# Optimization experiments

Measured on AMD Instinct MI355X. Metric: run time of the kernel, lower is better.

## Reference

```python
import jax, jax.numpy as jnp
import numpy as np

FEATURE_STRIDE = 16
CFG = {"TRAIN": dict(pre=12000, post=2000, thresh=0.7, min_size=16.0),
       "TEST":  dict(pre=6000,  post=300,  thresh=0.7, min_size=16.0)}

def _generate_anchors(base_size=16, ratios=(0.5, 1.0, 2.0), scales=(8, 16, 32)):
    xc = yc = (base_size - 1) * 0.5
    size = float(base_size * base_size)
    out = []
    for r in ratios:
        w = np.round(np.sqrt(size / r))
        h = np.round(w * r)
        for s in scales:
            W, H = w * s, h * s
            out.append([xc - 0.5 * (W - 1), yc - 0.5 * (H - 1),
                        xc + 0.5 * (W - 1), yc + 0.5 * (H - 1)])
    return np.array(out, np.float32)

ANCHORS = jnp.asarray(_generate_anchors())  # (9, 4)
NUM_ANCHORS = ANCHORS.shape[0]

def _pairwise_iou(b):
    x1, y1, x2, y2 = b[:, 0], b[:, 1], b[:, 2], b[:, 3]
    area = (x2 - x1 + 1.0) * (y2 - y1 + 1.0)
    iw = jnp.clip(jnp.minimum(x2[:, None], x2[None]) - jnp.maximum(x1[:, None], x1[None]) + 1.0, 0.0)
    ih = jnp.clip(jnp.minimum(y2[:, None], y2[None]) - jnp.maximum(y1[:, None], y1[None]) + 1.0, 0.0)
    inter = iw * ih
    return inter / (area[:, None] + area[None] - inter)

def _nms_keep(boxes, valid, thresh):
    # greedy NMS over score-sorted boxes; returns bool keep mask
    K = boxes.shape[0]
    iou = _pairwise_iou(boxes)  # (K, K)
    rng = jnp.arange(K)
    def body(i, keep):
        conflict = jnp.any((rng < i) & keep & (iou[i] > thresh))
        return keep.at[i].set(valid[i] & ~conflict)
    return jax.lax.fori_loop(0, K, body, jnp.zeros((K,), bool))

def reference(rpn_cls_scores, rpn_bbox_adjusts, img_shapes, train):
    cfg = CFG["TRAIN" if train else "TEST"]
    B, _, H, W = rpn_cls_scores.shape
    A = NUM_ANCHORS
    # fg scores: channels [A:2A], layout (h, w, a) after permute
    scores = rpn_cls_scores[:, A:].transpose(0, 2, 3, 1).reshape(B, -1)      # (B, N)
    deltas = rpn_bbox_adjusts.transpose(0, 2, 3, 1).reshape(B, -1, 4)        # (B, N, 4)
    # all anchors on the feature grid
    sx = jnp.arange(W, dtype=jnp.float32) * FEATURE_STRIDE
    sy = jnp.arange(H, dtype=jnp.float32) * FEATURE_STRIDE
    gy, gx = jnp.meshgrid(sy, sx, indexing="ij")
    shifts = jnp.stack([gx, gy, gx, gy], -1).reshape(-1, 4)                  # (H*W, 4)
    anchors = (shifts[:, None, :] + ANCHORS[None]).reshape(-1, 4)            # (N, 4)
    # bbox_transform_inv (+1 convention)
    aw = anchors[:, 2] - anchors[:, 0] + 1.0
    ah = anchors[:, 3] - anchors[:, 1] + 1.0
    acx = anchors[:, 0] + 0.5 * aw
    acy = anchors[:, 1] + 0.5 * ah
    pcx = deltas[..., 0] * aw + acx
    pcy = deltas[..., 1] * ah + acy
    pw = jnp.exp(deltas[..., 2]) * aw
    ph = jnp.exp(deltas[..., 3]) * ah
    x1, y1 = pcx - 0.5 * pw, pcy - 0.5 * ph
    x2, y2 = pcx + 0.5 * pw, pcy + 0.5 * ph
    imh, imw = img_shapes[:, 0:1], img_shapes[:, 1:2]
    x1 = jnp.clip(x1, 0.0, imw - 1.0); x2 = jnp.clip(x2, 0.0, imw - 1.0)
    y1 = jnp.clip(y1, 0.0, imh - 1.0); y2 = jnp.clip(y2, 0.0, imh - 1.0)
    boxes = jnp.stack([x1, y1, x2, y2], -1)                                  # (B, N, 4)
    valid = ((x2 - x1 + 1.0) >= cfg["min_size"]) & ((y2 - y1 + 1.0) >= cfg["min_size"])
    masked = jnp.where(valid, scores, -jnp.inf)
    K = min(cfg["pre"], boxes.shape[1])
    top_s, idx = jax.lax.top_k(masked, K)                                    # (B, K)
    top_b = jnp.take_along_axis(boxes, idx[..., None], axis=1)               # (B, K, 4)
    keep = jax.vmap(lambda b, v: _nms_keep(b, v, cfg["thresh"]))(
        jax.lax.stop_gradient(top_b), jnp.isfinite(top_s))
    post = cfg["post"]
    fin_s = jnp.where(keep, top_s, -jnp.inf)
    sel_s, idx2 = jax.lax.top_k(fin_s, post)
    sel_b = jnp.take_along_axis(top_b, idx2[..., None], axis=1)              # (B, post, 4)
    sel_b = jnp.where(jnp.isfinite(sel_s)[..., None], sel_b, 0.0)
    bix = jnp.broadcast_to(jnp.arange(B, dtype=sel_b.dtype)[:, None, None], (B, post, 1))
    return jnp.concatenate([bix, sel_b], -1)                                 # (B, post, 5)

def setup_inputs():
    key = jax.random.key(0)
    k1, k2 = jax.random.split(key)
    B, H, W = 4, 64, 96
    rpn_cls_scores = jax.random.normal(k1, (B, 2 * NUM_ANCHORS, H, W), jnp.float32)
    rpn_bbox_adjusts = jax.random.normal(k2, (B, 4 * NUM_ANCHORS, H, W), jnp.float32) * 0.1
    img_shapes = jnp.tile(jnp.array([[1024.0, 1536.0]], jnp.float32), (B, 1))
    return {"rpn_cls_scores": rpn_cls_scores, "rpn_bbox_adjusts": rpn_bbox_adjusts,
            "img_shapes": img_shapes, "train": 0}
```

## Files before the change

### kernel.cpp

```cpp
#include <hip/hip_runtime.h>


#define NB 4
#define AH 64
#define AW 96
#define NA 9
#define NPOS (AH*AW)
#define NPC (NPOS*NA)
#define CAP 16384
#define PREMAX 12000
#define POSTMAX 2048
#define HSZ 65536

__constant__ float c_anchors[NA][4] = {
  { -84.f,  -40.f,  99.f,  55.f},
  {-176.f,  -88.f, 191.f, 103.f},
  {-360.f, -184.f, 375.f, 199.f},
  { -56.f,  -56.f,  71.f,  71.f},
  {-120.f, -120.f, 135.f, 135.f},
  {-248.f, -248.f, 263.f, 263.f},
  { -36.f,  -80.f,  51.f,  95.f},
  { -80.f, -168.f,  95.f, 183.f},
  {-168.f, -344.f, 183.f, 359.f},
};

__device__ unsigned int       g_keys[NB][NPC];
__device__ float4             g_boxes[NB][NPC];
__device__ unsigned int       g_h16[NB][HSZ];
__device__ unsigned int       g_pivot[NB];
__device__ int                g_cnt[NB];
__device__ unsigned long long g_cand[NB][CAP];
__device__ int                g_cidx[NB][CAP];
__device__ int                g_rank[NB][CAP];
__device__ float4             g_sbox[NB][PREMAX];

__device__ __forceinline__ bool iou_gt(float4 a, float areaA, float4 q, float areaQ) {
#pragma clang fp contract(off)
  float iw = fminf(a.z, q.z) - fmaxf(a.x, q.x) + 1.0f; iw = fmaxf(iw, 0.0f);
  float ih = fminf(a.w, q.w) - fmaxf(a.y, q.y) + 1.0f; ih = fmaxf(ih, 0.0f);
  float inter = iw * ih;
  float denom = areaA + areaQ - inter;
  float d = inter - 0.7f * denom;
  if (__builtin_expect(fabsf(d) <= 4e-6f * denom, 0))
    return (inter / denom) > 0.7f;
  return d > 0.0f;
}

__global__ void __launch_bounds__(256) k_decode(const float* __restrict__ cls,
                                                const float* __restrict__ dlt,
                                                const float* __restrict__ ish) {
#pragma clang fp contract(off)
  int b   = blockIdx.y;
  int a   = blockIdx.x / (NPOS/256);
  int pos = (blockIdx.x % (NPOS/256)) * 256 + threadIdx.x;
  int wx  = pos % AW;
  int hy  = pos / AW;

  float score = cls[(b * (2*NA) + NA + a) * NPOS + pos];
  const float* dp = dlt + (b * (4*NA) + a*4) * NPOS + pos;
  float d0 = dp[0];
  float d1 = dp[NPOS];
  float d2 = dp[2*NPOS];
  float d3 = dp[3*NPOS];

  float shx = (float)(wx * 16);
  float shy = (float)(hy * 16);
  float ax1 = c_anchors[a][0] + shx;
  float ay1 = c_anchors[a][1] + shy;
  float ax2 = c_anchors[a][2] + shx;
  float ay2 = c_anchors[a][3] + shy;

  float aw_ = ax2 - ax1 + 1.0f;
  float ah_ = ay2 - ay1 + 1.0f;
  float acx = ax1 + 0.5f * aw_;
  float acy = ay1 + 0.5f * ah_;

  float pcx = d0 * aw_ + acx;
  float pcy = d1 * ah_ + acy;
  float pw  = expf(d2) * aw_;
  float ph  = expf(d3) * ah_;

  float x1 = pcx - 0.5f * pw;
  float y1 = pcy - 0.5f * ph;
  float x2 = pcx + 0.5f * pw;
  float y2 = pcy + 0.5f * ph;

  float imh = ish[b*2 + 0];
  float imw = ish[b*2 + 1];
  x1 = fminf(fmaxf(x1, 0.0f), imw - 1.0f);
  x2 = fminf(fmaxf(x2, 0.0f), imw - 1.0f);
  y1 = fminf(fmaxf(y1, 0.0f), imh - 1.0f);
  y2 = fminf(fmaxf(y2, 0.0f), imh - 1.0f);

  bool valid = ((x2 - x1 + 1.0f) >= 16.0f) && ((y2 - y1 + 1.0f) >= 16.0f);

  int i2 = a * NPOS + pos;
  g_boxes[b][i2] = make_float4(x1, y1, x2, y2);

  unsigned int key = 0u;
  if (valid) {
    unsigned int ub = __float_as_uint(score);
    key = (ub >> 31) ? ~ub : (ub | 0x80000000u);
  }
  g_keys[b][i2] = key;
  atomicAdd(&g_h16[b][key >> 16], 1u);
}

__global__ void __launch_bounds__(256) k_pivot(const int* __restrict__ train) {
  int b = blockIdx.x;
  int tid = threadIdx.x;
  unsigned int pre = train[0] ? 12000u : 6000u;
  const int CH = HSZ / 256;
  __shared__ unsigned int csum[256];
  __shared__ unsigned int csuf[257];
  __shared__ int best;

  uint4* hp = (uint4*)&g_h16[b][tid * CH];
  unsigned int s = 0;
#pragma unroll
  for (int q = 0; q < CH/4; ++q) { uint4 v = hp[q]; s += v.x + v.y + v.z + v.w; }
  csum[tid] = s;
  if (tid == 0) { best = 0; g_cnt[b] = 0; }
  __syncthreads();
  if (tid == 0) {
    unsigned int run = 0;
    csuf[256] = 0;
    for (int c = 255; c >= 0; --c) { run += csum[c]; csuf[c] = run; }
  }
  __syncthreads();

  unsigned int run = csuf[tid + 1];
  int loc = 0;
  for (int q = CH - 1; q >= 0; --q) {
    run += g_h16[b][tid * CH + q];
    if (loc == 0 && run >= pre) {
      int T = tid * CH + q;
      if (T >= 1) loc = T;
    }
  }
  uint4 z = make_uint4(0u, 0u, 0u, 0u);
#pragma unroll
  for (int q = 0; q < CH/4; ++q) hp[q] = z;

  if (loc) atomicMax(&best, loc);
  __syncthreads();
  if (tid == 0)
    g_pivot[b] = best ? ((unsigned int)best << 16) : 1u;
}

__global__ void __launch_bounds__(256) k_compact() {
  int b = blockIdx.y;
  int a   = blockIdx.x / (NPOS/256);
  int pos = (blockIdx.x % (NPOS/256)) * 256 + threadIdx.x;
  int i2 = a * NPOS + pos;
  unsigned int key = g_keys[b][i2];
  if (key >= g_pivot[b]) {
    int p = atomicAdd(&g_cnt[b], 1);
    if (p < CAP) {
      unsigned int iref = (unsigned int)(pos * NA + a);
      g_cand[b][p] = ((unsigned long long)key << 32) |
                     (unsigned long long)(0xFFFFFFFFu - iref);
      g_cidx[b][p] = i2;
    }
  }
}

__global__ void __launch_bounds__(256) k_rank() {
  int tid = threadIdx.x;
  __shared__ unsigned long long tl[256];
  for (int b = 0; b < NB; ++b) {
    int Cb = g_cnt[b]; if (Cb > CAP) Cb = CAP;
    int nt = (Cb + 255) >> 8;
    int tiles = nt * nt;
    for (int t = blockIdx.x; t < tiles; t += gridDim.x) {
      int jt = t / nt, kt = t - jt * nt;
      int k = kt * 256 + tid;
      tl[tid] = (k < Cb) ? g_cand[b][k] : 0ull;
      __syncthreads();
      int j = jt * 256 + tid;
      unsigned long long cj = (j < Cb) ? g_cand[b][j] : ~0ull;
      int r = 0;
#pragma unroll 8
      for (int q = 0; q < 256; ++q) r += (int)(tl[q] > cj);
      if (j < Cb && r) atomicAdd(&g_rank[b][j], r);
      __syncthreads();
    }
  }
}

__global__ void __launch_bounds__(512)
k_nms(float* __restrict__ out, const int* __restrict__ train, int post) {
#pragma clang fp contract(off)
  int b = blockIdx.x;
  int tid = threadIdx.x;
  int lane = tid & 63;
  int wid = tid >> 6;
  int pre = train[0] ? 12000 : 6000;
  int Cb = g_cnt[b]; if (Cb > CAP) Cb = CAP;
  int Kb = min(pre, Cb);

  for (int j = tid; j < Cb; j += 512) {
    int r = g_rank[b][j];
    g_rank[b][j] = 0;
    if (r < pre) {
      int i2 = g_cidx[b][j];
      g_sbox[b][r] = g_boxes[b][i2];
    }
  }
  __threadfence_block();
  __syncthreads();

  __shared__ float4 kbox[POSTMAX];
  __shared__ float  kar [POSTMAX];
  __shared__ float4 cbox[64];
  __shared__ float  car [64];
  __shared__ unsigned long long sup8[8];
  __shared__ unsigned long long conf8[8][64];
  __shared__ int s_nk;
  if (tid == 0) s_nk = 0;
  __syncthreads();
  int nk = 0;

  unsigned long long laneBitsBelow = (lane == 0) ? 0ull : (~0ull >> (64 - lane));

  for (int base = 0; base < Kb; base += 64) {
    int c = base + lane;
    bool active = (c < Kb);
    float4 bx = active ? g_sbox[b][c] : make_float4(0.f, 0.f, -1.f, -1.f);
    float area = (bx.z - bx.x + 1.0f) * (bx.w - bx.y + 1.0f);
    if (wid == 0) { cbox[lane] = bx; car[lane] = area; }

    int supp = active ? 0 : 1;
    {
      int t = wid;
      for (; t + 24 < nk; t += 32) {
        supp |= (int)iou_gt(bx, area, kbox[t],    kar[t]);
        supp |= (int)iou_gt(bx, area, kbox[t+8],  kar[t+8]);
        supp |= (int)iou_gt(bx, area, kbox[t+16], kar[t+16]);
        supp |= (int)iou_gt(bx, area, kbox[t+24], kar[t+24]);
      }
      for (; t < nk; t += 8) supp |= (int)iou_gt(bx, area, kbox[t], kar[t]);
    }
    unsigned long long myb = __ballot(supp);
    if (lane == 0) sup8[wid] = myb;
    __syncthreads();

    {
      unsigned long long confp = 0ull;
#pragma unroll
      for (int q = 0; q < 8; ++q) {
        int j = wid * 8 + q;
        if (iou_gt(bx, area, cbox[j], car[j])) confp |= (1ull << j);
      }
      conf8[wid][lane] = confp;
    }
    __syncthreads();

    if (wid == 0) {
      unsigned long long conf = (conf8[0][lane] | conf8[1][lane] |
                                 conf8[2][lane] | conf8[3][lane] |
                                 conf8[4][lane] | conf8[5][lane] |
                                 conf8[6][lane] | conf8[7][lane]) & laneBitsBelow;
      unsigned long long supAll = sup8[0] | sup8[1] | sup8[2] | sup8[3] |
                                  sup8[4] | sup8[5] | sup8[6] | sup8[7];
      unsigned long long pending = ~supAll;
      unsigned long long keptmask = 0ull;
      while (pending) {
        int i = __ffsll(pending) - 1;
        keptmask |= (1ull << i);
        unsigned long long confb = __ballot((int)((conf >> i) & 1ull));
        pending &= ~confb;
        pending &= ~(1ull << i);
      }
      int myPos = nk + __popcll(keptmask & laneBitsBelow);
      if (((keptmask >> lane) & 1ull) && myPos < post) {
        kbox[myPos] = bx;
        kar [myPos] = area;
        float* o = out + ((size_t)b * post + myPos) * 5;
        o[0] = (float)b; o[1] = bx.x; o[2] = bx.y; o[3] = bx.z; o[4] = bx.w;
      }
      if (lane == 0) s_nk = nk + __popcll(keptmask);
    }
    __syncthreads();
    nk = s_nk;
    if (nk >= post) break;
  }

  nk = min(nk, post);
  for (int r = nk + tid; r < post; r += 512) {
    float* o = out + ((size_t)b * post + r) * 5;
    o[0] = (float)b; o[1] = 0.0f; o[2] = 0.0f; o[3] = 0.0f; o[4] = 0.0f;
  }
}

extern "C" void kernel_launch(void* const* d_in, const int* in_sizes, int n_in,
                              void* d_out, int out_size, void* d_ws, size_t ws_size,
                              hipStream_t stream) {
  const float* cls   = (const float*)d_in[0];
  const float* dlt   = (const float*)d_in[1];
  const float* ish   = (const float*)d_in[2];
  const int*   train = (const int*)d_in[3];
  float* out = (float*)d_out;

  int post = out_size / (NB * 5);

  dim3 gdec(NA * (NPOS/256), NB);
  k_decode<<<gdec, 256, 0, stream>>>(cls, dlt, ish);

  k_pivot<<<NB, 256, 0, stream>>>(train);

  k_compact<<<gdec, 256, 0, stream>>>();

  k_rank<<<1024, 256, 0, stream>>>();

  k_nms<<<NB, 512, 0, stream>>>(out, train, post);
}
```

Before: 195.8 us.

## Fuse all proposal stages into one persistent kernel with grid barriers

Replaces the five launches (decode, pivot, compact, rank, NMS) with a single persistent kernel of 256 blocks of 1024 threads that move between stages through global atomic spin barriers. Alongside this, the histogram shrinks from 16 to 15 bits, the rank tiles grow, and NMS runs with 16 waves while the next 64-box chunk is prefetched. The aim is to remove launch gaps and widen the NMS stage. The risks are deadlock if all 256 blocks are not co-resident, the cost of the spin barriers themselves, and a serial NMS tail that still runs on only four blocks.

```diff
diff --git a/kernel.cpp b/kernel.cpp
--- a/kernel.cpp
+++ b/kernel.cpp
@@ -10,7 +10,12 @@
 #define CAP 16384
 #define PREMAX 12000
 #define POSTMAX 2048
-#define HSZ 65536
+#define HBITS 15
+#define HSZ (1<<HBITS)
+#define HSH (32-HBITS)
+#define NBLK 256
+#define NTHR 1024
+#define UNITS (NB*NA*(NPOS/NTHR))
 
 __constant__ float c_anchors[NA][4] = {
   { -84.f,  -40.f,  99.f,  55.f},
@@ -26,13 +31,26 @@
 
 __device__ unsigned int       g_keys[NB][NPC];
 __device__ float4             g_boxes[NB][NPC];
-__device__ unsigned int       g_h16[NB][HSZ];
+__device__ unsigned int       g_h15[NB][HSZ];
 __device__ unsigned int       g_pivot[NB];
 __device__ int                g_cnt[NB];
 __device__ unsigned long long g_cand[NB][CAP];
 __device__ int                g_cidx[NB][CAP];
 __device__ int                g_rank[NB][CAP];
 __device__ float4             g_sbox[NB][PREMAX];
+__device__ unsigned int       g_bar[8];
+
+__device__ __forceinline__ void gbar(int k) {
+  __syncthreads();
+  if (threadIdx.x == 0) {
+    __threadfence();
+    atomicAdd(&g_bar[k], 1u);
+    while (atomicAdd(&g_bar[k], 0u) < (unsigned)NBLK)
+      __builtin_amdgcn_s_sleep(8);
+    __threadfence();
+  }
+  __syncthreads();
+}
 
 __device__ __forceinline__ bool iou_gt(float4 a, float areaA, float4 q, float areaQ) {
 #pragma clang fp contract(off)
@@ -46,256 +64,295 @@
   return d > 0.0f;
 }
 
-__global__ void __launch_bounds__(256) k_decode(const float* __restrict__ cls,
-                                                const float* __restrict__ dlt,
-                                                const float* __restrict__ ish) {
+__global__ void __launch_bounds__(NTHR)
+k_all(const float* __restrict__ cls, const float* __restrict__ dlt,
+      const float* __restrict__ ish, const int* __restrict__ train,
+      float* __restrict__ out, int post) {
 #pragma clang fp contract(off)
-  int b   = blockIdx.y;
-  int a   = blockIdx.x / (NPOS/256);
-  int pos = (blockIdx.x % (NPOS/256)) * 256 + threadIdx.x;
-  int wx  = pos % AW;
-  int hy  = pos / AW;
-
-  float score = cls[(b * (2*NA) + NA + a) * NPOS + pos];
-  const float* dp = dlt + (b * (4*NA) + a*4) * NPOS + pos;
-  float d0 = dp[0];
-  float d1 = dp[NPOS];
-  float d2 = dp[2*NPOS];
-  float d3 = dp[3*NPOS];
-
-  float shx = (float)(wx * 16);
-  float shy = (float)(hy * 16);
-  float ax1 = c_anchors[a][0] + shx;
-  float ay1 = c_anchors[a][1] + shy;
-  float ax2 = c_anchors[a][2] + shx;
-  float ay2 = c_anchors[a][3] + shy;
-
-  float aw_ = ax2 - ax1 + 1.0f;
-  float ah_ = ay2 - ay1 + 1.0f;
-  float acx = ax1 + 0.5f * aw_;
-  float acy = ay1 + 0.5f * ah_;
-
-  float pcx = d0 * aw_ + acx;
-  float pcy = d1 * ah_ + acy;
-  float pw  = expf(d2) * aw_;
-  float ph  = expf(d3) * ah_;
-
-  float x1 = pcx - 0.5f * pw;
-  float y1 = pcy - 0.5f * ph;
-  float x2 = pcx + 0.5f * pw;
-  float y2 = pcy + 0.5f * ph;
-
-  float imh = ish[b*2 + 0];
-  float imw = ish[b*2 + 1];
-  x1 = fminf(fmaxf(x1, 0.0f), imw - 1.0f);
-  x2 = fminf(fmaxf(x2, 0.0f), imw - 1.0f);
-  y1 = fminf(fmaxf(y1, 0.0f), imh - 1.0f);
-  y2 = fminf(fmaxf(y2, 0.0f), imh - 1.0f);
-
-  bool valid = ((x2 - x1 + 1.0f) >= 16.0f) && ((y2 - y1 + 1.0f) >= 16.0f);
-
-  int i2 = a * NPOS + pos;
-  g_boxes[b][i2] = make_float4(x1, y1, x2, y2);
-
-  unsigned int key = 0u;
-  if (valid) {
-    unsigned int ub = __float_as_uint(score);
-    key = (ub >> 31) ? ~ub : (ub | 0x80000000u);
-  }
-  g_keys[b][i2] = key;
-  atomicAdd(&g_h16[b][key >> 16], 1u);
-}
-
-__global__ void __launch_bounds__(256) k_pivot(const int* __restrict__ train) {
-  int b = blockIdx.x;
-  int tid = threadIdx.x;
-  unsigned int pre = train[0] ? 12000u : 6000u;
-  const int CH = HSZ / 256;
-  __shared__ unsigned int csum[256];
-  __shared__ unsigned int csuf[257];
-  __shared__ int best;
-
-  uint4* hp = (uint4*)&g_h16[b][tid * CH];
-  unsigned int s = 0;
-#pragma unroll
-  for (int q = 0; q < CH/4; ++q) { uint4 v = hp[q]; s += v.x + v.y + v.z + v.w; }
-  csum[tid] = s;
-  if (tid == 0) { best = 0; g_cnt[b] = 0; }
-  __syncthreads();
-  if (tid == 0) {
-    unsigned int run = 0;
-    csuf[256] = 0;
-    for (int c = 255; c >= 0; --c) { run += csum[c]; csuf[c] = run; }
-  }
-  __syncthreads();
-
-  unsigned int run = csuf[tid + 1];
-  int loc = 0;
-  for (int q = CH - 1; q >= 0; --q) {
-    run += g_h16[b][tid * CH + q];
-    if (loc == 0 && run >= pre) {
-      int T = tid * CH + q;
-      if (T >= 1) loc = T;
-    }
-  }
-  uint4 z = make_uint4(0u, 0u, 0u, 0u);
-#pragma unroll
-  for (int q = 0; q < CH/4; ++q) hp[q] = z;
-
-  if (loc) atomicMax(&best, loc);
-  __syncthreads();
-  if (tid == 0)
-    g_pivot[b] = best ? ((unsigned int)best << 16) : 1u;
-}
-
-__global__ void __launch_bounds__(256) k_compact() {
-  int b = blockIdx.y;
-  int a   = blockIdx.x / (NPOS/256);
-  int pos = (blockIdx.x % (NPOS/256)) * 256 + threadIdx.x;
-  int i2 = a * NPOS + pos;
-  unsigned int key = g_keys[b][i2];
-  if (key >= g_pivot[b]) {
-    int p = atomicAdd(&g_cnt[b], 1);
-    if (p < CAP) {
-      unsigned int iref = (unsigned int)(pos * NA + a);
-      g_cand[b][p] = ((unsigned long long)key << 32) |
-                     (unsigned long long)(0xFFFFFFFFu - iref);
-      g_cidx[b][p] = i2;
-    }
-  }
-}
-
-__global__ void __launch_bounds__(256) k_rank() {
-  int tid = threadIdx.x;
-  __shared__ unsigned long long tl[256];
-  for (int b = 0; b < NB; ++b) {
-    int Cb = g_cnt[b]; if (Cb > CAP) Cb = CAP;
-    int nt = (Cb + 255) >> 8;
-    int tiles = nt * nt;
-    for (int t = blockIdx.x; t < tiles; t += gridDim.x) {
-      int jt = t / nt, kt = t - jt * nt;
-      int k = kt * 256 + tid;
-      tl[tid] = (k < Cb) ? g_cand[b][k] : 0ull;
-      __syncthreads();
-      int j = jt * 256 + tid;
-      unsigned long long cj = (j < Cb) ? g_cand[b][j] : ~0ull;
-      int r = 0;
-#pragma unroll 8
-      for (int q = 0; q < 256; ++q) r += (int)(tl[q] > cj);
-      if (j < Cb && r) atomicAdd(&g_rank[b][j], r);
-      __syncthreads();
-    }
-  }
-}
-
-__global__ void __launch_bounds__(512)
-k_nms(float* __restrict__ out, const int* __restrict__ train, int post) {
-#pragma clang fp contract(off)
-  int b = blockIdx.x;
-  int tid = threadIdx.x;
-  int lane = tid & 63;
-  int wid = tid >> 6;
-  int pre = train[0] ? 12000 : 6000;
-  int Cb = g_cnt[b]; if (Cb > CAP) Cb = CAP;
-  int Kb = min(pre, Cb);
-
-  for (int j = tid; j < Cb; j += 512) {
-    int r = g_rank[b][j];
-    g_rank[b][j] = 0;
-    if (r < pre) {
-      int i2 = g_cidx[b][j];
-      g_sbox[b][r] = g_boxes[b][i2];
-    }
-  }
-  __threadfence_block();
-  __syncthreads();
+  const int tid = threadIdx.x;
+  const int bid = blockIdx.x;
+  const int pre = train[0] ? 12000 : 6000;
 
   __shared__ float4 kbox[POSTMAX];
   __shared__ float  kar [POSTMAX];
   __shared__ float4 cbox[64];
   __shared__ float  car [64];
-  __shared__ unsigned long long sup8[8];
-  __shared__ unsigned long long conf8[8][64];
+  __shared__ unsigned long long conf16[16][64];
+  __shared__ unsigned long long sup16[16];
   __shared__ int s_nk;
-  if (tid == 0) s_nk = 0;
+  __shared__ unsigned int csum[NTHR];
+  __shared__ unsigned int c32[32];
+  __shared__ unsigned int c32s[33];
+  __shared__ int sBest;
+  __shared__ unsigned long long tl[256];
+
+  for (int u = bid; u < UNITS; u += NBLK) {
+    int b  = u / (NA * (NPOS/NTHR));
+    int r  = u % (NA * (NPOS/NTHR));
+    int a  = r / (NPOS/NTHR);
+    int pos = (r % (NPOS/NTHR)) * NTHR + tid;
+    int wx = pos % AW;
+    int hy = pos / AW;
+
+    float score = cls[(b * (2*NA) + NA + a) * NPOS + pos];
+    const float* dp = dlt + (b * (4*NA) + a*4) * NPOS + pos;
+    float d0 = dp[0];
+    float d1 = dp[NPOS];
+    float d2 = dp[2*NPOS];
+    float d3 = dp[3*NPOS];
+
+    float shx = (float)(wx * 16);
+    float shy = (float)(hy * 16);
+    float ax1 = c_anchors[a][0] + shx;
+    float ay1 = c_anchors[a][1] + shy;
+    float ax2 = c_anchors[a][2] + shx;
+    float ay2 = c_anchors[a][3] + shy;
+
+    float aw_ = ax2 - ax1 + 1.0f;
+    float ah_ = ay2 - ay1 + 1.0f;
+    float acx = ax1 + 0.5f * aw_;
+    float acy = ay1 + 0.5f * ah_;
+
+    float pcx = d0 * aw_ + acx;
+    float pcy = d1 * ah_ + acy;
+    float pw  = expf(d2) * aw_;
+    float ph  = expf(d3) * ah_;
+
+    float x1 = pcx - 0.5f * pw;
+    float y1 = pcy - 0.5f * ph;
+    float x2 = pcx + 0.5f * pw;
+    float y2 = pcy + 0.5f * ph;
+
+    float imh = ish[b*2 + 0];
+    float imw = ish[b*2 + 1];
+    x1 = fminf(fmaxf(x1, 0.0f), imw - 1.0f);
+    x2 = fminf(fmaxf(x2, 0.0f), imw - 1.0f);
+    y1 = fminf(fmaxf(y1, 0.0f), imh - 1.0f);
+    y2 = fminf(fmaxf(y2, 0.0f), imh - 1.0f);
+
+    bool valid = ((x2 - x1 + 1.0f) >= 16.0f) && ((y2 - y1 + 1.0f) >= 16.0f);
+
+    int i2 = a * NPOS + pos;
+    g_boxes[b][i2] = make_float4(x1, y1, x2, y2);
+
+    unsigned int key = 0u;
+    if (valid) {
+      unsigned int ub = __float_as_uint(score);
+      key = (ub >> 31) ? ~ub : (ub | 0x80000000u);
+    }
+    g_keys[b][i2] = key;
+    atomicAdd(&g_h15[b][key >> HSH], 1u);
+  }
+  gbar(0);
+
+  if (bid < NB) {
+    int b = bid;
+    const int CH = HSZ / NTHR;
+    unsigned int hb[CH];
+    const uint4* hp = (const uint4*)&g_h15[b][tid * CH];
+#pragma unroll
+    for (int q = 0; q < CH/4; ++q) {
+      uint4 v = hp[q];
+      hb[4*q+0] = v.x; hb[4*q+1] = v.y; hb[4*q+2] = v.z; hb[4*q+3] = v.w;
+    }
+    unsigned int s = 0;
+#pragma unroll
+    for (int q = 0; q < CH; ++q) s += hb[q];
+    csum[tid] = s;
+    if (tid == 0) { sBest = 0; g_cnt[b] = 0; }
+    __syncthreads();
+    if (tid < 32) {
+      unsigned int ss = 0;
+      for (int q = 0; q < 32; ++q) ss += csum[tid*32 + q];
+      c32[tid] = ss;
+    }
+    __syncthreads();
+    if (tid == 0) {
+      unsigned int run = 0; c32s[32] = 0;
+      for (int c = 31; c >= 0; --c) { run += c32[c]; c32s[c] = run; }
+    }
+    __syncthreads();
+    unsigned int run = c32s[(tid >> 5) + 1];
+    for (int t2 = (tid | 31); t2 > tid; --t2) run += csum[t2];
+    int loc = 0;
+#pragma unroll
+    for (int q = CH-1; q >= 0; --q) {
+      run += hb[q];
+      if (!loc && run >= (unsigned)pre) {
+        int T = tid * CH + q;
+        if (T >= 1) loc = T;
+      }
+    }
+    uint4 z = make_uint4(0u,0u,0u,0u);
+    uint4* hpw = (uint4*)&g_h15[b][tid * CH];
+#pragma unroll
+    for (int q = 0; q < CH/4; ++q) hpw[q] = z;
+
+    if (loc) atomicMax(&sBest, loc);
+    __syncthreads();
+    if (tid == 0)
+      g_pivot[b] = sBest ? ((unsigned int)sBest << HSH) : 1u;
+  }
+  gbar(1);
+
+  for (int u = bid; u < UNITS; u += NBLK) {
+    int b  = u / (NA * (NPOS/NTHR));
+    int r  = u % (NA * (NPOS/NTHR));
+    int a  = r / (NPOS/NTHR);
+    int pos = (r % (NPOS/NTHR)) * NTHR + tid;
+    int i2 = a * NPOS + pos;
+    unsigned int key = g_keys[b][i2];
+    if (key >= g_pivot[b]) {
+      int p = atomicAdd(&g_cnt[b], 1);
+      if (p < CAP) {
+        unsigned int iref = (unsigned int)(pos * NA + a);
+        g_cand[b][p] = ((unsigned long long)key << 32) |
+                       (unsigned long long)(0xFFFFFFFFu - iref);
+        g_cidx[b][p] = i2;
+      }
+    }
+  }
+  gbar(2);
+
+  for (int b = 0; b < NB; ++b) {
+    int C = g_cnt[b]; if (C > CAP) C = CAP;
+    int ntJ = (C + NTHR-1) >> 10;
+    int ntK = (C + 255) >> 8;
+    int jobs = ntJ * ntK;
+    for (int t = bid; t < jobs; t += NBLK) {
+      int jt = t / ntK, kt = t - jt * ntK;
+      if (tid < 256) {
+        int k = kt * 256 + tid;
+        tl[tid] = (k < C) ? g_cand[b][k] : 0ull;
+      }
+      __syncthreads();
+      int j = jt * NTHR + tid;
+      unsigned long long cj = (j < C) ? g_cand[b][j] : ~0ull;
+      int rk = 0;
+#pragma unroll 8
+      for (int q = 0; q < 256; ++q) rk += (int)(tl[q] > cj);
+      if (j < C && rk) atomicAdd(&g_rank[b][j], rk);
+      __syncthreads();
+    }
+  }
+  gbar(3);
+
+  if (bid < NB) {
+    int b = bid;
+    int lane = tid & 63;
+    int wid  = tid >> 6;
+    int Cb = g_cnt[b]; if (Cb > CAP) Cb = CAP;
+    int Kb = min(pre, Cb);
+
+    for (int j = tid; j < Cb; j += NTHR) {
+      int r = g_rank[b][j];
+      g_rank[b][j] = 0;
+      if (r < pre) g_sbox[b][r] = g_boxes[b][g_cidx[b][j]];
+    }
+    if (tid == 0) s_nk = 0;
+    __syncthreads();
+
+    if (wid == 15) {
+      float4 bx0 = (lane < Kb) ? g_sbox[b][lane] : make_float4(0.f,0.f,-1.f,-1.f);
+      cbox[lane] = bx0;
+      car[lane]  = (bx0.z - bx0.x + 1.0f) * (bx0.w - bx0.y + 1.0f);
+    }
+    __syncthreads();
+
+    int nk = 0;
+    unsigned long long laneBitsBelow = (lane == 0) ? 0ull : (~0ull >> (64 - lane));
+
+    for (int base = 0; base < Kb; base += 64) {
+      float4 bx  = cbox[lane];
+      float area = car[lane];
+      bool active = (base + lane < Kb);
+
+      float4 nxt = make_float4(0.f, 0.f, -1.f, -1.f);
+      if (wid == 15) {
+        int c2 = base + 64 + lane;
+        if (c2 < Kb) nxt = g_sbox[b][c2];
+      }
+
+      int supp = active ? 0 : 1;
+      {
+        int t = wid;
+        for (; t + 48 < nk; t += 64) {
+          supp |= (int)iou_gt(bx, area, kbox[t],    kar[t]);
+          supp |= (int)iou_gt(bx, area, kbox[t+16], kar[t+16]);
+          supp |= (int)iou_gt(bx, area, kbox[t+32], kar[t+32]);
+          supp |= (int)iou_gt(bx, area, kbox[t+48], kar[t+48]);
+        }
+        for (; t < nk; t += 16) supp |= (int)iou_gt(bx, area, kbox[t], kar[t]);
+      }
+      unsigned long long sb = __ballot(supp);
+      if (lane == 0) sup16[wid] = sb;
+
+      {
+        unsigned long long confp = 0ull;
+#pragma unroll
+        for (int q = 0; q < 4; ++q) {
+          int j = (wid << 2) + q;
+          if (iou_gt(bx, area, cbox[j], car[j])) confp |= (1ull << j);
+        }
+        conf16[wid][lane] = confp;
+      }
+      __syncthreads();
+
+      if (wid == 0) {
+        unsigned long long conf = 0ull;
+#pragma unroll
+        for (int w = 0; w < 16; ++w) conf |= conf16[w][lane];
+        conf &= laneBitsBelow;
+        unsigned long long supAll = 0ull;
+#pragma unroll
+        for (int w = 0; w < 16; ++w) supAll |= sup16[w];
+        unsigned long long pending = ~supAll;
+        unsigned long long keptmask = 0ull;
+        while (pending) {
+          int i = __ffsll(pending) - 1;
+          keptmask |= (1ull << i);
+          unsigned long long confb = __ballot((int)((conf >> i) & 1ull));
+          pending &= ~confb;
+          pending &= ~(1ull << i);
+        }
+        int myPos = nk + __popcll(keptmask & laneBitsBelow);
+        if (((keptmask >> lane) & 1ull) && myPos < post) {
+          kbox[myPos] = bx;
+          kar [myPos] = area;
+          float* o = out + ((size_t)b * post + myPos) * 5;
+          o[0] = (float)b; o[1] = bx.x; o[2] = bx.y; o[3] = bx.z; o[4] = bx.w;
+        }
+        if (lane == 0) s_nk = nk + __popcll(keptmask);
+      } else if (wid == 15) {
+        cbox[lane] = nxt;
+        car[lane]  = (nxt.z - nxt.x + 1.0f) * (nxt.w - nxt.y + 1.0f);
+      }
+      __syncthreads();
+      nk = s_nk;
+      if (nk >= post) break;
+    }
+
+    nk = min(nk, post);
+    for (int r = nk + tid; r < post; r += NTHR) {
+      float* o = out + ((size_t)b * post + r) * 5;
+      o[0] = (float)b; o[1] = 0.0f; o[2] = 0.0f; o[3] = 0.0f; o[4] = 0.0f;
+    }
+  }
+
   __syncthreads();
-  int nk = 0;
-
-  unsigned long long laneBitsBelow = (lane == 0) ? 0ull : (~0ull >> (64 - lane));
-
-  for (int base = 0; base < Kb; base += 64) {
-    int c = base + lane;
-    bool active = (c < Kb);
-    float4 bx = active ? g_sbox[b][c] : make_float4(0.f, 0.f, -1.f, -1.f);
-    float area = (bx.z - bx.x + 1.0f) * (bx.w - bx.y + 1.0f);
-    if (wid == 0) { cbox[lane] = bx; car[lane] = area; }
-
-    int supp = active ? 0 : 1;
-    {
-      int t = wid;
-      for (; t + 24 < nk; t += 32) {
-        supp |= (int)iou_gt(bx, area, kbox[t],    kar[t]);
-        supp |= (int)iou_gt(bx, area, kbox[t+8],  kar[t+8]);
-        supp |= (int)iou_gt(bx, area, kbox[t+16], kar[t+16]);
-        supp |= (int)iou_gt(bx, area, kbox[t+24], kar[t+24]);
-      }
-      for (; t < nk; t += 8) supp |= (int)iou_gt(bx, area, kbox[t], kar[t]);
-    }
-    unsigned long long myb = __ballot(supp);
-    if (lane == 0) sup8[wid] = myb;
-    __syncthreads();
-
-    {
-      unsigned long long confp = 0ull;
-#pragma unroll
-      for (int q = 0; q < 8; ++q) {
-        int j = wid * 8 + q;
-        if (iou_gt(bx, area, cbox[j], car[j])) confp |= (1ull << j);
-      }
-      conf8[wid][lane] = confp;
-    }
-    __syncthreads();
-
-    if (wid == 0) {
-      unsigned long long conf = (conf8[0][lane] | conf8[1][lane] |
-                                 conf8[2][lane] | conf8[3][lane] |
-                                 conf8[4][lane] | conf8[5][lane] |
-                                 conf8[6][lane] | conf8[7][lane]) & laneBitsBelow;
-      unsigned long long supAll = sup8[0] | sup8[1] | sup8[2] | sup8[3] |
-                                  sup8[4] | sup8[5] | sup8[6] | sup8[7];
-      unsigned long long pending = ~supAll;
-      unsigned long long keptmask = 0ull;
-      while (pending) {
-        int i = __ffsll(pending) - 1;
-        keptmask |= (1ull << i);
-        unsigned long long confb = __ballot((int)((conf >> i) & 1ull));
-        pending &= ~confb;
-        pending &= ~(1ull << i);
-      }
-      int myPos = nk + __popcll(keptmask & laneBitsBelow);
-      if (((keptmask >> lane) & 1ull) && myPos < post) {
-        kbox[myPos] = bx;
-        kar [myPos] = area;
-        float* o = out + ((size_t)b * post + myPos) * 5;
-        o[0] = (float)b; o[1] = bx.x; o[2] = bx.y; o[3] = bx.z; o[4] = bx.w;
-      }
-      if (lane == 0) s_nk = nk + __popcll(keptmask);
-    }
-    __syncthreads();
-    nk = s_nk;
-    if (nk >= post) break;
-  }
-
-  nk = min(nk, post);
-  for (int r = nk + tid; r < post; r += 512) {
-    float* o = out + ((size_t)b * post + r) * 5;
-    o[0] = (float)b; o[1] = 0.0f; o[2] = 0.0f; o[3] = 0.0f; o[4] = 0.0f;
+  if (tid == 0) {
+    __threadfence();
+    unsigned int p = atomicAdd(&g_bar[4], 1u);
+    if (p == (unsigned)(NBLK - 1)) {
+      for (int k = 0; k < 8; ++k) atomicExch(&g_bar[k], 0u);
+    }
   }
 }
 
 extern "C" void kernel_launch(void* const* d_in, const int* in_sizes, int n_in,
                               void* d_out, int out_size, void* d_ws, size_t ws_size,
                               hipStream_t stream) {
+  (void)in_sizes; (void)n_in; (void)d_ws; (void)ws_size;
   const float* cls   = (const float*)d_in[0];
   const float* dlt   = (const float*)d_in[1];
   const float* ish   = (const float*)d_in[2];
@@ -304,14 +361,5 @@
 
   int post = out_size / (NB * 5);
 
-  dim3 gdec(NA * (NPOS/256), NB);
-  k_decode<<<gdec, 256, 0, stream>>>(cls, dlt, ish);
-
-  k_pivot<<<NB, 256, 0, stream>>>(train);
-
-  k_compact<<<gdec, 256, 0, stream>>>();
-
-  k_rank<<<1024, 256, 0, stream>>>();
-
-  k_nms<<<NB, 512, 0, stream>>>(out, train, post);
+  k_all<<<NBLK, NTHR, 0, stream>>>(cls, dlt, ish, train, out, post);
 }
```

After: 233.2 us. +19.1%, slower.
